# Kernel tuning notes

Hardware: AMD Instinct MI355X
Metric: run time of the kernel (lower is better)

## Reference

```python
import jax, jax.numpy as jnp
import numpy as np

E, D_MODEL, D_FF = 8, 1024, 4096
B, S = 4, 2048


def setup_inputs() -> dict:
    key = jax.random.key(0)
    ks = jax.random.split(key, 7)
    scale_in = 1.0 / np.sqrt(D_MODEL)
    scale_ff = 1.0 / np.sqrt(D_FF)
    return {
        "x": jax.random.normal(ks[0], (B, S, D_MODEL), dtype=jnp.float32),
        "w1": jax.random.normal(ks[1], (E, D_MODEL, D_FF), dtype=jnp.float32) * scale_in,
        "b1": jax.random.normal(ks[2], (E, D_FF), dtype=jnp.float32) * 0.01,
        "w2": jax.random.normal(ks[3], (E, D_FF, D_MODEL), dtype=jnp.float32) * scale_ff,
        "b2": jax.random.normal(ks[4], (E, D_MODEL), dtype=jnp.float32) * 0.01,
        "gate_w": jax.random.normal(ks[5], (D_MODEL, E), dtype=jnp.float32) * scale_in,
        "gate_b": jax.random.normal(ks[6], (E,), dtype=jnp.float32) * 0.01,
    }


def reference(x, w1, b1, w2, b2, gate_w, gate_b):
    # Gating: softmax then top-1 (argmax of probs == argmax of logits)
    gate_logits = x @ gate_w + gate_b                      # [B,S,E]
    gate_probs = jax.nn.softmax(gate_logits, axis=-1)
    top1 = jnp.argmax(gate_probs, axis=-1)                 # [B,S] int
    mask = jax.nn.one_hot(top1, E, dtype=x.dtype)          # [B,S,E]

    # Dense compute of every expert on every token (faithful to source)
    h = jax.nn.relu(jnp.einsum('bsd,edf->ebsf', x, w1) + b1[:, None, None, :])  # [E,B,S,F]
    y = jnp.einsum('ebsf,efd->ebsd', h, w2) + b2[:, None, None, :]              # [E,B,S,D]

    # Top-1 mask-and-sum combine (note: no gate-prob scaling in the original)
    out = jnp.einsum('ebsd,bse->bsd', y, mask)             # [B,S,D]
    return out
```

## Files before the change

kernel.cpp:

```cpp
#include <hip/hip_runtime.h>
#include <stdint.h>

#define DM 1024
#define DF 4096
#define NE 8
#define NTOK 8192
#define MT256 40

typedef __attribute__((ext_vector_type(8))) short short8;
typedef __attribute__((ext_vector_type(8))) unsigned short ushort8v;
typedef __attribute__((ext_vector_type(4))) float floatx4;

__device__ inline unsigned short f2bf(float f) {
    union { float f; unsigned u; } v; v.f = f;
    unsigned u = v.u;
    u += 0x7fffu + ((u >> 16) & 1u);
    return (unsigned short)(u >> 16);
}

#define GLDS(g, l) __builtin_amdgcn_global_load_lds( \
    (const __attribute__((address_space(1))) void*)(g), \
    (__attribute__((address_space(3))) void*)(l), 16, 0, 0)

#define VMW(N)  asm volatile("s_waitcnt vmcnt(" #N ")" ::: "memory")
#define LGKM0   asm volatile("s_waitcnt lgkmcnt(0)" ::: "memory")
#define SCHED0  __builtin_amdgcn_sched_barrier(0)
#define BAR     __builtin_amdgcn_s_barrier()

__global__ void gate_kernel(const float* __restrict__ x, const float* __restrict__ gw,
                            const float* __restrict__ gb, int* __restrict__ top1,
                            unsigned short* __restrict__ xb) {
    int t = blockIdx.x;
    int lane = threadIdx.x;
    const float* xr = x + (size_t)t * DM;
    unsigned short* xbr = xb + (size_t)t * DM;
    double acc[NE];
#pragma unroll
    for (int e = 0; e < NE; ++e) acc[e] = 0.0;
    for (int j = 0; j < DM / 64; ++j) {
        int d = j * 64 + lane;
        float xf = xr[d];
        xbr[d] = f2bf(xf);
        double xv = (double)xf;
        const float* g = gw + (size_t)d * NE;
#pragma unroll
        for (int e = 0; e < NE; ++e) acc[e] = fma(xv, (double)g[e], acc[e]);
    }
#pragma unroll
    for (int e = 0; e < NE; ++e) {
        for (int off = 32; off > 0; off >>= 1)
            acc[e] += __shfl_down(acc[e], off, 64);
    }
    if (lane == 0) {
        int best = 0;
        double bv = acc[0] + (double)gb[0];
        for (int e = 1; e < NE; ++e) {
            double v = acc[e] + (double)gb[e];
            if (v > bv) { bv = v; best = e; }
        }
        top1[t] = best;
    }
}

__global__ void count_kernel(const int* __restrict__ top1, int* __restrict__ ctrl) {
    int t = blockIdx.x * 256 + threadIdx.x;
    int e = top1[t];
    int lane = threadIdx.x & 63;
#pragma unroll
    for (int ex = 0; ex < NE; ++ex) {
        unsigned long long m = __ballot(e == ex);
        if (m != 0ull && lane == (__ffsll((long long)m) - 1))
            atomicAdd(&ctrl[ex], __popcll(m));
    }
}

__global__ void prefix_kernel(int* ctrl) {
    if (threadIdx.x == 0) {
        int s = 0, t256 = 0;
        for (int e = 0; e < NE; ++e) {
            int cnt = ctrl[e];
            ctrl[8 + e] = s; ctrl[17 + e] = s;
            for (int m = 0; m * 256 < cnt; ++m) {
                ctrl[32 + 3 * t256] = e;
                ctrl[33 + 3 * t256] = s + m * 256;
                int rr = cnt - m * 256;
                ctrl[34 + 3 * t256] = rr < 256 ? rr : 256;
                ++t256;
            }
            s += cnt;
        }
        ctrl[16] = s;
        ctrl[25] = t256;
    }
}

__global__ void scatter_kernel(const int* __restrict__ top1, int* __restrict__ ctrl,
                               int* __restrict__ perm) {
    int t = blockIdx.x * 256 + threadIdx.x;
    int e = top1[t];
    int lane = threadIdx.x & 63;
#pragma unroll
    for (int ex = 0; ex < NE; ++ex) {
        unsigned long long m = __ballot(e == ex);
        if (m == 0ull) continue;
        int leader = __ffsll((long long)m) - 1;
        int base = 0;
        if (lane == leader) base = atomicAdd(&ctrl[17 + ex], __popcll(m));
        base = __shfl(base, leader, 64);
        if (e == ex) {
            int pos = __popcll(m & ((1ull << lane) - 1ull));
            perm[base + pos] = t;
        }
    }
}

__global__ void transpose_both(const float* __restrict__ w1, unsigned short* __restrict__ w1t,
                               const float* __restrict__ w2, unsigned short* __restrict__ w2t) {
    constexpr int NT1 = NE * (DM / 64) * (DF / 64);
    __shared__ float tile[64][65];
    int bid = blockIdx.x;
    const float* src; unsigned short* dst; int R, C;
    if (bid < NT1) { src = w1; dst = w1t; R = DM; C = DF; }
    else           { bid -= NT1; src = w2; dst = w2t; R = DF; C = DM; }
    int tilesR = R >> 6, tilesC = C >> 6;
    int e = bid / (tilesR * tilesC);
    int rem = bid % (tilesR * tilesC);
    int tr = rem / tilesC, tc = rem % tilesC;
    const float* s = src + (size_t)e * R * C + (size_t)(tr * 64) * C + tc * 64;
    unsigned short* d = dst + (size_t)e * R * C + (size_t)(tc * 64) * R + tr * 64;
    int tid = threadIdx.x;
#pragma unroll
    for (int i = 0; i < 4; ++i) {
        int idx = i * 256 + tid;
        int r = idx >> 4, c4 = (idx & 15) * 4;
        float4 v = *(const float4*)(s + (size_t)r * C + c4);
        tile[r][c4 + 0] = v.x; tile[r][c4 + 1] = v.y;
        tile[r][c4 + 2] = v.z; tile[r][c4 + 3] = v.w;
    }
    __syncthreads();
#pragma unroll
    for (int i = 0; i < 2; ++i) {
        int idx = i * 256 + tid;
        int c = idx >> 3, r8 = (idx & 7) * 8;
        ushort8v o;
#pragma unroll
        for (int j = 0; j < 8; ++j) o[j] = f2bf(tile[r8 + j][c]);
        *(ushort8v*)(d + (size_t)c * R + r8) = o;
    }
}

#define F_SLAB(u, SU, STG, W) do { \
    if (STG) { \
        int kk_ = ((SU) + 3) * 32; \
        GLDS(ap0 + kk_, &As[((u) + 3) & 3][(size_t)tid * 8]); \
        GLDS(ap1 + kk_, &As[((u) + 3) & 3][(size_t)(512 + tid) * 8]); \
        GLDS(bp0 + kk_, &Bs[((u) + 3) & 3][(size_t)tid * 8]); \
        GLDS(bp1 + kk_, &Bs[((u) + 3) & 3][(size_t)(512 + tid) * 8]); \
    } \
    short8 af[8], bf[4]; \
    _Pragma("unroll") \
    for (int m_ = 0; m_ < 8; ++m_) af[m_] = *(const short8*)&As[u][aoff[m_]]; \
    _Pragma("unroll") \
    for (int n_ = 0; n_ < 4; ++n_) bf[n_] = *(const short8*)&Bs[u][boff[n_]]; \
    LGKM0; SCHED0; \
    __builtin_amdgcn_s_setprio(1); \
    _Pragma("unroll") \
    for (int m_ = 0; m_ < 8; ++m_) \
        _Pragma("unroll") \
        for (int n_ = 0; n_ < 4; ++n_) \
            acc[m_][n_] = __builtin_amdgcn_mfma_f32_16x16x32_bf16(af[m_], bf[n_], acc[m_][n_], 0, 0, 0); \
    __builtin_amdgcn_s_setprio(0); \
    W; SCHED0; BAR; \
} while (0)

template<bool FFN1>
__global__ __launch_bounds__(512, 2) void ffn_gemm(
    const unsigned short* __restrict__ A,
    const unsigned short* __restrict__ Bt,
    const float* __restrict__ bias,
    const int* __restrict__ ctrl,
    const int* __restrict__ perm,
    unsigned short* __restrict__ Hout,
    float* __restrict__ Yout) {
    constexpr int K = FFN1 ? DM : DF;
    constexpr int N = FFN1 ? DF : DM;
    constexpr int NT = N / 256;
    constexpr int NKI = K / 32;
    constexpr int SLABSZ = 256 * 32;
    constexpr int G = 8;

    int nwg = gridDim.x;
    int bo = blockIdx.x;
    int q = nwg >> 3, r = nwg & 7;
    int xcd = bo & 7, lid = bo >> 3;
    int b = (xcd < r ? xcd * (q + 1) : r * (q + 1) + (xcd - r) * q) + lid;

    int grp = b / (G * NT);
    int ii = b % (G * NT);
    int nt = ii / G;
    int til = grp * G + (ii % G);
    if (til >= ctrl[25]) return;
    int e       = ctrl[32 + 3 * til];
    int rowbase = ctrl[33 + 3 * til];
    int rows    = ctrl[34 + 3 * til];

    __shared__ __align__(16) unsigned short As[4][SLABSZ];
    __shared__ __align__(16) unsigned short Bs[4][SLABSZ];

    int tid = threadIdx.x, lane = tid & 63, wave = tid >> 6;
    int wm = (wave >> 2) * 128;
    int wn = (wave & 3) * 64;

    int rA0 = tid >> 2, rA1 = 128 + (tid >> 2);
    int kofs = ((tid & 3) ^ ((tid >> 3) & 3)) * 8;
    int c0 = rowbase + (rA0 < rows ? rA0 : rows - 1);
    int c1 = rowbase + (rA1 < rows ? rA1 : rows - 1);
    const unsigned short* ap0;
    const unsigned short* ap1;
    if (FFN1) {
        ap0 = A + (size_t)perm[c0] * K + kofs;
        ap1 = A + (size_t)perm[c1] * K + kofs;
    } else {
        ap0 = A + (size_t)c0 * K + kofs;
        ap1 = A + (size_t)c1 * K + kofs;
    }
    const unsigned short* bb  = Bt + (size_t)e * N * K + (size_t)(nt * 256) * K + kofs;
    const unsigned short* bp0 = bb + (size_t)rA0 * K;
    const unsigned short* bp1 = bb + (size_t)rA1 * K;

    int aoff[8], boff[4];
#pragma unroll
    for (int m = 0; m < 8; ++m) {
        int R = wm + m * 16 + (lane & 15);
        aoff[m] = R * 32 + (((lane >> 4) ^ ((R >> 1) & 3)) * 8);
    }
#pragma unroll
    for (int n = 0; n < 4; ++n) {
        int R = wn + n * 16 + (lane & 15);
        boff[n] = R * 32 + (((lane >> 4) ^ ((R >> 1) & 3)) * 8);
    }

    floatx4 acc[8][4];
#pragma unroll
    for (int i = 0; i < 8; ++i)
#pragma unroll
        for (int j = 0; j < 4; ++j) acc[i][j] = floatx4{0.f, 0.f, 0.f, 0.f};

#pragma unroll
    for (int s = 0; s < 3; ++s) {
        GLDS(ap0 + s * 32, &As[s][(size_t)tid * 8]);
        GLDS(ap1 + s * 32, &As[s][(size_t)(512 + tid) * 8]);
        GLDS(bp0 + s * 32, &Bs[s][(size_t)tid * 8]);
        GLDS(bp1 + s * 32, &Bs[s][(size_t)(512 + tid) * 8]);
    }
    VMW(8); SCHED0; BAR;

#pragma unroll 1
    for (int s = 0; s < NKI - 4; s += 4) {
        F_SLAB(0, s + 0, 1, VMW(8));
        F_SLAB(1, s + 1, 1, VMW(8));
        F_SLAB(2, s + 2, 1, VMW(8));
        F_SLAB(3, s + 3, 1, VMW(8));
    }
    F_SLAB(0, NKI - 4, 1, VMW(8));
    F_SLAB(1, NKI - 3, 0, VMW(4));
    F_SLAB(2, NKI - 2, 0, VMW(0));
    F_SLAB(3, NKI - 1, 0, (void)0);

    int col0 = nt * 256 + wn + (lane & 15);
    int rowq = (lane >> 4) * 4;
    float bv[4];
#pragma unroll
    for (int n = 0; n < 4; ++n) bv[n] = bias[e * N + col0 + n * 16];

#pragma unroll
    for (int m = 0; m < 8; ++m) {
#pragma unroll
        for (int r2 = 0; r2 < 4; ++r2) {
            int lr = wm + m * 16 + rowq + r2;
            if (lr < rows) {
                if (FFN1) {
                    unsigned short* hr = Hout + (size_t)(rowbase + lr) * DF + col0;
#pragma unroll
                    for (int n = 0; n < 4; ++n) {
                        float v = acc[m][n][r2] + bv[n];
                        v = v > 0.f ? v : 0.f;
                        hr[n * 16] = f2bf(v);
                    }
                } else {
                    float* yr = Yout + (size_t)perm[rowbase + lr] * DM + col0;
#pragma unroll
                    for (int n = 0; n < 4; ++n)
                        yr[n * 16] = acc[m][n][r2] + bv[n];
                }
            }
        }
    }
}
#undef F_SLAB

extern "C" void kernel_launch(void* const* d_in, const int* in_sizes, int n_in,
                              void* d_out, int out_size, void* d_ws, size_t ws_size,
                              hipStream_t stream) {
    const float* x  = (const float*)d_in[0];
    const float* w1 = (const float*)d_in[1];
    const float* b1 = (const float*)d_in[2];
    const float* w2 = (const float*)d_in[3];
    const float* b2 = (const float*)d_in[4];
    const float* gw = (const float*)d_in[5];
    const float* gb = (const float*)d_in[6];
    float* out = (float*)d_out;

    char* ws = (char*)d_ws;
    int* ctrl = (int*)ws;
    int* top1 = (int*)(ws + 2048);
    int* perm = (int*)(ws + 2048 + 32768);
    size_t o = 67584;
    unsigned short* xb  = (unsigned short*)(ws + o);        o += (size_t)NTOK * DM * 2;
    unsigned short* w1t = (unsigned short*)(ws + o);        o += (size_t)NE * DM * DF * 2;
    unsigned short* w2t = (unsigned short*)(ws + o);        o += (size_t)NE * DM * DF * 2;
    unsigned short* H   = (unsigned short*)(ws + o);

    hipMemsetAsync(ctrl, 0, 2048, stream);
    gate_kernel<<<NTOK, 64, 0, stream>>>(x, gw, gb, top1, xb);
    count_kernel<<<NTOK / 256, 256, 0, stream>>>(top1, ctrl);
    prefix_kernel<<<1, 64, 0, stream>>>(ctrl);
    scatter_kernel<<<NTOK / 256, 256, 0, stream>>>(top1, ctrl, perm);
    transpose_both<<<2 * NE * (DM / 64) * (DF / 64), 256, 0, stream>>>(w1, w1t, w2, w2t);
    ffn_gemm<true ><<<MT256 * (DF / 256), 512, 0, stream>>>(xb, w1t, b1, ctrl, perm, H, nullptr);
    ffn_gemm<false><<<MT256 * (DM / 256), 512, 0, stream>>>(H, w2t, b2, ctrl, perm, nullptr, out);
}
```

Baseline: 585.8 us.

## Fuse gate with weight transpose, merge routing into one sort kernel, split MFMA LDS reads

Gating now runs in the same launch as the weight transpose, with four tokens per block. The separate count, prefix and scatter kernels and the memset are replaced by a single 1024-thread block that counts, prefixes and scatters in shared memory. In the GEMM inner slab, A fragments are loaded in two halves and the explicit lgkmcnt(0) wait is removed, so the compiler can overlap LDS reads with MFMAs. This cuts launch overhead and small-kernel serialization, but the fused grid is heterogeneous and the sort runs on a single block.

New measurement: 562.0 us. -4.1%, faster.

```diff
diff --git a/kernel.cpp b/kernel.cpp
--- a/kernel.cpp
+++ b/kernel.cpp
@@ -23,102 +23,55 @@
     (__attribute__((address_space(3))) void*)(l), 16, 0, 0)
 
 #define VMW(N)  asm volatile("s_waitcnt vmcnt(" #N ")" ::: "memory")
-#define LGKM0   asm volatile("s_waitcnt lgkmcnt(0)" ::: "memory")
 #define SCHED0  __builtin_amdgcn_sched_barrier(0)
 #define BAR     __builtin_amdgcn_s_barrier()
 
-__global__ void gate_kernel(const float* __restrict__ x, const float* __restrict__ gw,
-                            const float* __restrict__ gb, int* __restrict__ top1,
-                            unsigned short* __restrict__ xb) {
-    int t = blockIdx.x;
-    int lane = threadIdx.x;
-    const float* xr = x + (size_t)t * DM;
-    unsigned short* xbr = xb + (size_t)t * DM;
-    double acc[NE];
-#pragma unroll
-    for (int e = 0; e < NE; ++e) acc[e] = 0.0;
-    for (int j = 0; j < DM / 64; ++j) {
-        int d = j * 64 + lane;
-        float xf = xr[d];
-        xbr[d] = f2bf(xf);
-        double xv = (double)xf;
-        const float* g = gw + (size_t)d * NE;
-#pragma unroll
-        for (int e = 0; e < NE; ++e) acc[e] = fma(xv, (double)g[e], acc[e]);
-    }
-#pragma unroll
-    for (int e = 0; e < NE; ++e) {
-        for (int off = 32; off > 0; off >>= 1)
-            acc[e] += __shfl_down(acc[e], off, 64);
-    }
-    if (lane == 0) {
-        int best = 0;
-        double bv = acc[0] + (double)gb[0];
-        for (int e = 1; e < NE; ++e) {
-            double v = acc[e] + (double)gb[e];
-            if (v > bv) { bv = v; best = e; }
-        }
-        top1[t] = best;
-    }
-}
-
-__global__ void count_kernel(const int* __restrict__ top1, int* __restrict__ ctrl) {
-    int t = blockIdx.x * 256 + threadIdx.x;
-    int e = top1[t];
-    int lane = threadIdx.x & 63;
-#pragma unroll
-    for (int ex = 0; ex < NE; ++ex) {
-        unsigned long long m = __ballot(e == ex);
-        if (m != 0ull && lane == (__ffsll((long long)m) - 1))
-            atomicAdd(&ctrl[ex], __popcll(m));
-    }
-}
-
-__global__ void prefix_kernel(int* ctrl) {
-    if (threadIdx.x == 0) {
-        int s = 0, t256 = 0;
-        for (int e = 0; e < NE; ++e) {
-            int cnt = ctrl[e];
-            ctrl[8 + e] = s; ctrl[17 + e] = s;
-            for (int m = 0; m * 256 < cnt; ++m) {
-                ctrl[32 + 3 * t256] = e;
-                ctrl[33 + 3 * t256] = s + m * 256;
-                int rr = cnt - m * 256;
-                ctrl[34 + 3 * t256] = rr < 256 ? rr : 256;
-                ++t256;
-            }
-            s += cnt;
-        }
-        ctrl[16] = s;
-        ctrl[25] = t256;
-    }
-}
-
-__global__ void scatter_kernel(const int* __restrict__ top1, int* __restrict__ ctrl,
-                               int* __restrict__ perm) {
-    int t = blockIdx.x * 256 + threadIdx.x;
-    int e = top1[t];
-    int lane = threadIdx.x & 63;
-#pragma unroll
-    for (int ex = 0; ex < NE; ++ex) {
-        unsigned long long m = __ballot(e == ex);
-        if (m == 0ull) continue;
-        int leader = __ffsll((long long)m) - 1;
-        int base = 0;
-        if (lane == leader) base = atomicAdd(&ctrl[17 + ex], __popcll(m));
-        base = __shfl(base, leader, 64);
-        if (e == ex) {
-            int pos = __popcll(m & ((1ull << lane) - 1ull));
-            perm[base + pos] = t;
-        }
-    }
-}
-
-__global__ void transpose_both(const float* __restrict__ w1, unsigned short* __restrict__ w1t,
-                               const float* __restrict__ w2, unsigned short* __restrict__ w2t) {
+__global__ __launch_bounds__(256) void gate_transpose(
+    const float* __restrict__ x, const float* __restrict__ gw, const float* __restrict__ gb,
+    int* __restrict__ top1, unsigned short* __restrict__ xb,
+    const float* __restrict__ w1, unsigned short* __restrict__ w1t,
+    const float* __restrict__ w2, unsigned short* __restrict__ w2t) {
+    constexpr int GATE_BLKS = NTOK / 4;
     constexpr int NT1 = NE * (DM / 64) * (DF / 64);
     __shared__ float tile[64][65];
     int bid = blockIdx.x;
+    int tid = threadIdx.x;
+
+    if (bid < GATE_BLKS) {
+        int wave = tid >> 6, lane = tid & 63;
+        int t = bid * 4 + wave;
+        const float* xr = x + (size_t)t * DM;
+        unsigned short* xbr = xb + (size_t)t * DM;
+        double acc[NE];
+#pragma unroll
+        for (int e = 0; e < NE; ++e) acc[e] = 0.0;
+        for (int j = 0; j < DM / 64; ++j) {
+            int d = j * 64 + lane;
+            float xf = xr[d];
+            xbr[d] = f2bf(xf);
+            double xv = (double)xf;
+            const float* g = gw + (size_t)d * NE;
+#pragma unroll
+            for (int e = 0; e < NE; ++e) acc[e] = fma(xv, (double)g[e], acc[e]);
+        }
+#pragma unroll
+        for (int e = 0; e < NE; ++e) {
+            for (int off = 32; off > 0; off >>= 1)
+                acc[e] += __shfl_down(acc[e], off, 64);
+        }
+        if (lane == 0) {
+            int best = 0;
+            double bv = acc[0] + (double)gb[0];
+            for (int e = 1; e < NE; ++e) {
+                double v = acc[e] + (double)gb[e];
+                if (v > bv) { bv = v; best = e; }
+            }
+            top1[t] = best;
+        }
+        return;
+    }
+
+    bid -= GATE_BLKS;
     const float* src; unsigned short* dst; int R, C;
     if (bid < NT1) { src = w1; dst = w1t; R = DM; C = DF; }
     else           { bid -= NT1; src = w2; dst = w2t; R = DF; C = DM; }
@@ -128,7 +81,6 @@
     int tr = rem / tilesC, tc = rem % tilesC;
     const float* s = src + (size_t)e * R * C + (size_t)(tr * 64) * C + tc * 64;
     unsigned short* d = dst + (size_t)e * R * C + (size_t)(tc * 64) * R + tr * 64;
-    int tid = threadIdx.x;
 #pragma unroll
     for (int i = 0; i < 4; ++i) {
         int idx = i * 256 + tid;
@@ -146,6 +98,64 @@
 #pragma unroll
         for (int j = 0; j < 8; ++j) o[j] = f2bf(tile[r8 + j][c]);
         *(ushort8v*)(d + (size_t)c * R + r8) = o;
+    }
+}
+
+__global__ __launch_bounds__(1024) void sort_kernel(const int* __restrict__ top1,
+                                                    int* __restrict__ ctrl,
+                                                    int* __restrict__ perm) {
+    __shared__ int cnt[NE];
+    __shared__ int cur[NE];
+    int tid = threadIdx.x, lane = tid & 63;
+    if (tid < NE) cnt[tid] = 0;
+    __syncthreads();
+    int ev[8];
+#pragma unroll
+    for (int j = 0; j < 8; ++j) ev[j] = top1[j * 1024 + tid];
+#pragma unroll
+    for (int e = 0; e < NE; ++e) {
+        int c = 0;
+#pragma unroll
+        for (int j = 0; j < 8; ++j) {
+            unsigned long long m = __ballot(ev[j] == e);
+            c += __popcll(m);
+        }
+        if (lane == 0) atomicAdd(&cnt[e], c);
+    }
+    __syncthreads();
+    if (tid == 0) {
+        int s = 0, t256 = 0;
+        for (int e = 0; e < NE; ++e) {
+            int c = cnt[e];
+            cur[e] = s;
+            for (int m = 0; m * 256 < c; ++m) {
+                ctrl[32 + 3 * t256] = e;
+                ctrl[33 + 3 * t256] = s + m * 256;
+                int rr = c - m * 256;
+                ctrl[34 + 3 * t256] = rr < 256 ? rr : 256;
+                ++t256;
+            }
+            s += c;
+        }
+        ctrl[25] = t256;
+    }
+    __syncthreads();
+#pragma unroll
+    for (int j = 0; j < 8; ++j) {
+        int e = ev[j];
+#pragma unroll
+        for (int ex = 0; ex < NE; ++ex) {
+            unsigned long long m = __ballot(e == ex);
+            if (m == 0ull) continue;
+            int leader = __ffsll((long long)m) - 1;
+            int base = 0;
+            if (lane == leader) base = atomicAdd(&cur[ex], __popcll(m));
+            base = __shfl(base, leader, 64);
+            if (e == ex) {
+                int pos = __popcll(m & ((1ull << lane) - 1ull));
+                perm[base + pos] = j * 1024 + tid;
+            }
+        }
     }
 }
 
@@ -157,18 +167,24 @@
         GLDS(bp0 + kk_, &Bs[((u) + 3) & 3][(size_t)tid * 8]); \
         GLDS(bp1 + kk_, &Bs[((u) + 3) & 3][(size_t)(512 + tid) * 8]); \
     } \
-    short8 af[8], bf[4]; \
-    _Pragma("unroll") \
-    for (int m_ = 0; m_ < 8; ++m_) af[m_] = *(const short8*)&As[u][aoff[m_]]; \
+    short8 bf[4], af[4], ag[4]; \
     _Pragma("unroll") \
     for (int n_ = 0; n_ < 4; ++n_) bf[n_] = *(const short8*)&Bs[u][boff[n_]]; \
-    LGKM0; SCHED0; \
+    _Pragma("unroll") \
+    for (int m_ = 0; m_ < 4; ++m_) af[m_] = *(const short8*)&As[u][aoff[m_]]; \
+    _Pragma("unroll") \
+    for (int m_ = 0; m_ < 4; ++m_) ag[m_] = *(const short8*)&As[u][aoff[4 + m_]]; \
     __builtin_amdgcn_s_setprio(1); \
     _Pragma("unroll") \
-    for (int m_ = 0; m_ < 8; ++m_) \
+    for (int m_ = 0; m_ < 4; ++m_) \
         _Pragma("unroll") \
         for (int n_ = 0; n_ < 4; ++n_) \
             acc[m_][n_] = __builtin_amdgcn_mfma_f32_16x16x32_bf16(af[m_], bf[n_], acc[m_][n_], 0, 0, 0); \
+    _Pragma("unroll") \
+    for (int m_ = 0; m_ < 4; ++m_) \
+        _Pragma("unroll") \
+        for (int n_ = 0; n_ < 4; ++n_) \
+            acc[4 + m_][n_] = __builtin_amdgcn_mfma_f32_16x16x32_bf16(ag[m_], bf[n_], acc[4 + m_][n_], 0, 0, 0); \
     __builtin_amdgcn_s_setprio(0); \
     W; SCHED0; BAR; \
 } while (0)
@@ -321,12 +337,9 @@
     unsigned short* w2t = (unsigned short*)(ws + o);        o += (size_t)NE * DM * DF * 2;
     unsigned short* H   = (unsigned short*)(ws + o);
 
-    hipMemsetAsync(ctrl, 0, 2048, stream);
-    gate_kernel<<<NTOK, 64, 0, stream>>>(x, gw, gb, top1, xb);
-    count_kernel<<<NTOK / 256, 256, 0, stream>>>(top1, ctrl);
-    prefix_kernel<<<1, 64, 0, stream>>>(ctrl);
-    scatter_kernel<<<NTOK / 256, 256, 0, stream>>>(top1, ctrl, perm);
-    transpose_both<<<2 * NE * (DM / 64) * (DF / 64), 256, 0, stream>>>(w1, w1t, w2, w2t);
+    gate_transpose<<<NTOK / 4 + 2 * NE * (DM / 64) * (DF / 64), 256, 0, stream>>>(
+        x, gw, gb, top1, xb, w1, w1t, w2, w2t);
+    sort_kernel<<<1, 1024, 0, stream>>>(top1, ctrl, perm);
     ffn_gemm<true ><<<MT256 * (DF / 256), 512, 0, stream>>>(xb, w1t, b1, ctrl, perm, H, nullptr);
     ffn_gemm<false><<<MT256 * (DM / 256), 512, 0, stream>>>(H, w2t, b2, ctrl, perm, nullptr, out);
 }
```
